# Optimization experiments

Hardware: AMD Instinct MI355X
Metric: run time of the kernel (lower is better)

Reference implementation:

```python
import jax, jax.numpy as jnp
import numpy as np
from jax import lax

B, M, D, N = 256, 1024, 128, 26  # batch, seq_len, feat_dim, num_labels


def setup_inputs() -> dict:
    key = jax.random.key(0)
    k1, k2, k3, k4 = jax.random.split(key, 4)
    X = jax.random.normal(k1, (B, M, D), dtype=jnp.float32)
    labels = jax.random.randint(k2, (B, M), 0, N, dtype=jnp.int32)
    # Learned CRF params (zeros in the module; random here for a non-degenerate test).
    W = jax.random.normal(k3, (N, D), dtype=jnp.float32) * 0.05
    T = jax.random.normal(k4, (N, N), dtype=jnp.float32) * 0.1
    return {"X": X, "labels": labels, "W": W, "T": T}


def _seq_log_prob(x, y, W, T):
    # x: [M, D], y: [M] int labels.
    # Original forward_messages (prob space): f[i,a] = exp(x_i.W_a) * sum_b exp(T[b,a]) f[i-1,b]
    # Computed here equivalently in log space for numerical stability.
    e = x @ W.T  # [M, N] emission scores x_i . W_a

    def step(lf, e_i):
        # logsumexp over previous label b of (lf[b] + T[b, a])
        lf_new = e_i + jax.nn.logsumexp(lf[:, None] + T, axis=0)
        return lf_new, None

    lf_last, _ = lax.scan(step, e[0], e[1:])
    logZ = jax.nn.logsumexp(lf_last)
    unnorm = jnp.sum(jnp.take_along_axis(e, y[:, None], axis=1)) \
        + jnp.sum(T[y[:-1], y[1:]])
    return unnorm - logZ


def reference(X, labels, W, T):
    # CRF.forward with identity conv stack: mean log p(y | x) over the batch.
    log_probs = jax.vmap(lambda x, y: _seq_log_prob(x, y, W, T))(X, labels)
    return jnp.mean(log_probs)
```

## Files before the change

### kernel.cpp

```cpp
#include <hip/hip_runtime.h>

#define CB 256
#define CM 1024
#define CD 128
#define CN 26

typedef __attribute__((ext_vector_type(2))) float f32x2;

__device__ inline float rfl_f(float x) {
    return __int_as_float(__builtin_amdgcn_readfirstlane(__float_as_int(x)));
}
__device__ inline float rdl_f(float x, int lane) {
#if __has_builtin(__builtin_amdgcn_readlane)
    return __int_as_float(__builtin_amdgcn_readlane(__float_as_int(x), lane));
#else
    return __shfl(x, lane, 64);
#endif
}
__device__ inline float fexp2(float x) {
#if __has_builtin(__builtin_amdgcn_exp2f)
    return __builtin_amdgcn_exp2f(x);
#else
    return exp2f(x);
#endif
}
__device__ inline float flog2(float x) {
#if __has_builtin(__builtin_amdgcn_logf)
    return __builtin_amdgcn_logf(x);
#else
    return log2f(x);
#endif
}
__device__ inline f32x2 fma2(f32x2 a, f32x2 b, f32x2 c) {
#if __has_builtin(__builtin_elementwise_fma)
    return __builtin_elementwise_fma(a, b, c);
#else
    f32x2 r;
    r[0] = fmaf(a[0], b[0], c[0]);
    r[1] = fmaf(a[1], b[1], c[1]);
    return r;
#endif
}

__global__ __launch_bounds__(256, 2) void emit_kernel(
    const float* __restrict__ X, const float* __restrict__ W,
    const int* __restrict__ labels, const float* __restrict__ T,
    float* __restrict__ E, float* __restrict__ out) {
    const int t = threadIdx.x;
    const int row = blockIdx.x * 256 + t;
    const float4* __restrict__ x4 =
        reinterpret_cast<const float4*>(X + (size_t)row * CD);

    f32x2 acc2[CN];
#pragma unroll
    for (int a = 0; a < CN; ++a) acc2[a] = (f32x2){0.f, 0.f};

    f32x2 xa[8], xb[8];
#pragma unroll
    for (int q = 0; q < 4; ++q)
        *reinterpret_cast<float4*>(&xa[q * 2]) = x4[q];

#pragma unroll
    for (int c = 0; c < 8; ++c) {
        f32x2* cur = (c & 1) ? xb : xa;
        f32x2* nxt = (c & 1) ? xa : xb;
        if (c < 7) {
#pragma unroll
            for (int q = 0; q < 4; ++q)
                *reinterpret_cast<float4*>(&nxt[q * 2]) = x4[(c + 1) * 4 + q];
        }
#pragma unroll
        for (int a = 0; a < CN; ++a) {
            const f32x2* wp =
                reinterpret_cast<const f32x2*>(W + a * CD + c * 16);
#pragma unroll
            for (int jj = 0; jj < 8; ++jj)
                acc2[a] = fma2(cur[jj], wp[jj], acc2[a]);
        }
    }

    float acc[CN];
#pragma unroll
    for (int a = 0; a < CN; ++a) acc[a] = acc2[a][0] + acc2[a][1];

    const float LOG2E = 1.4426950408889634f;
    float2* e2 = reinterpret_cast<float2*>(E + (size_t)row * CN);
#pragma unroll
    for (int a = 0; a < CN / 2; ++a)
        e2[a] = make_float2(acc[2 * a] * LOG2E, acc[2 * a + 1] * LOG2E);

    int y = labels[row];
    float us = acc[0];
#pragma unroll
    for (int a = 1; a < CN; ++a) us = (y == a) ? acc[a] : us;
    if (row & (CM - 1)) {
        int yp = labels[row - 1];
        us += T[yp * CN + y];
    }
#pragma unroll
    for (int off = 32; off > 0; off >>= 1) us += __shfl_xor(us, off, 64);
    __shared__ float rsum[4];
    if ((t & 63) == 0) rsum[t >> 6] = us;
    __syncthreads();
    if (t == 0)
        atomicAdd(out, (rsum[0] + rsum[1] + rsum[2] + rsum[3]) * (1.f / CB));
}

template <bool BWD>
__device__ void run_half(float* __restrict__ base, const float* __restrict__ T,
                         int a, int l) {
    float AT[CN];
#pragma unroll
    for (int k = 0; k < CN; ++k)
        AT[k] = expf(BWD ? T[a * CN + k] : T[k * CN + a]);

    const int S = BWD ? -CN : CN;
    const float* __restrict__ Eb = base + (BWD ? (size_t)1023 * CN : 0) + a;

    float f, L = 0.f;
    float epf[8];
    const float* pf;
    if (BWD) {
        f = 1.f;
#pragma unroll
        for (int k = 0; k < 8; ++k) epf[k] = Eb[k * S];
        pf = Eb + 8 * S;
    } else {
        f = fexp2(Eb[0]);
#pragma unroll
        for (int k = 0; k < 8; ++k) epf[k] = Eb[(1 + k) * S];
        pf = Eb + 9 * S;
    }

    auto step = [&](float e_cur, bool renorm) {
        float p = fexp2(e_cur);
        float x = BWD ? p * f : f;
        float d0 = 0.f, d1 = 0.f, d2 = 0.f, d3 = 0.f;
#pragma unroll
        for (int b = 0; b < 24; b += 4) {
            d0 = fmaf(AT[b + 0], rdl_f(x, b + 0), d0);
            d1 = fmaf(AT[b + 1], rdl_f(x, b + 1), d1);
            d2 = fmaf(AT[b + 2], rdl_f(x, b + 2), d2);
            d3 = fmaf(AT[b + 3], rdl_f(x, b + 3), d3);
        }
        d0 = fmaf(AT[24], rdl_f(x, 24), d0);
        d1 = fmaf(AT[25], rdl_f(x, 25), d1);
        float d = (d0 + d1) + (d2 + d3);
        f = BWD ? d : p * d;
        if (renorm) {
            float fr = rfl_f(f);
            int k2 = (int)((__float_as_uint(fr) >> 23) & 255) - 127;
            f = ldexpf(f, -k2);
            L += (float)k2;
        }
    };

    const int NMAIN = BWD ? 63 : 62;
    for (int it = 0; it < NMAIN; ++it) {
#pragma unroll
        for (int k = 0; k < 8; ++k) {
            float e_cur = epf[k];
            epf[k] = pf[k * S];
            step(e_cur, k == 7);
        }
        pf += 8 * S;
    }
    if (BWD) {
#pragma unroll
        for (int k = 0; k < 8; ++k) step(epf[k], k == 7);
    } else {
#pragma unroll
        for (int k = 0; k < 8; ++k) {
            float e_cur = epf[k];
            if (k < 7) epf[k] = pf[k * S];
            step(e_cur, k == 7);
        }
#pragma unroll
        for (int k = 0; k < 7; ++k) step(epf[k], false);
    }

    {
        float fr = rfl_f(f);
        int k2 = (int)((__float_as_uint(fr) >> 23) & 255) - 127;
        f = ldexpf(f, -k2);
        L += (float)k2;
    }

    base[(BWD ? (size_t)1023 * CN : 0) + a] = f;
    if (l == 0) base[(BWD ? (size_t)1022 * CN : (size_t)CN)] = L;
}

__global__ __launch_bounds__(64) void crf_half_kernel(
    float* __restrict__ E, const float* __restrict__ T) {
    const int s = blockIdx.x >> 1;
    const int l = threadIdx.x;
    const int a = (l < CN) ? l : (CN - 1);
    float* base = E + (size_t)s * CM * CN;
    if (blockIdx.x & 1)
        run_half<true>(base, T, a, l);
    else
        run_half<false>(base, T, a, l);
}

__global__ __launch_bounds__(64) void crf_combine_kernel(
    const float* __restrict__ E, float* __restrict__ out) {
    const int s = blockIdx.x;
    const int l = threadIdx.x;
    const float LN2 = 0.6931471805599453f;
    const float* base = E + (size_t)s * CM * CN;

    float v = 0.f;
    if (l < CN) v = base[l] * base[(size_t)1023 * CN + l];
#pragma unroll
    for (int off = 32; off > 0; off >>= 1) v += __shfl_xor(v, off, 64);

    if (l == 0) {
        float Lf = base[CN];
        float Lb = base[(size_t)1022 * CN];
        float logZ = LN2 * (Lf + Lb + flog2(v));
        atomicAdd(out, -logZ * (1.f / (float)CB));
    }
}

extern "C" void kernel_launch(void* const* d_in, const int* in_sizes, int n_in,
                              void* d_out, int out_size, void* d_ws,
                              size_t ws_size, hipStream_t stream) {
    const float* X = (const float*)d_in[0];
    const int* labels = (const int*)d_in[1];
    const float* W = (const float*)d_in[2];
    const float* T = (const float*)d_in[3];
    float* out = (float*)d_out;
    float* E = (float*)d_ws;

    hipMemsetAsync(d_out, 0, sizeof(float), stream);
    emit_kernel<<<(CB * CM) / 256, 256, 0, stream>>>(X, W, labels, T, E, out);
    crf_half_kernel<<<CB * 2, 64, 0, stream>>>(E, T);
    crf_combine_kernel<<<CB, 64, 0, stream>>>(E, out);
}
```

Measured before the change: 294.8 us.

## Stage W in LDS and compute four rows per thread in emission kernel

```diff
diff --git a/kernel.cpp b/kernel.cpp
--- a/kernel.cpp
+++ b/kernel.cpp
@@ -4,8 +4,6 @@
 #define CM 1024
 #define CD 128
 #define CN 26
-
-typedef __attribute__((ext_vector_type(2))) float f32x2;
 
 __device__ inline float rfl_f(float x) {
     return __int_as_float(__builtin_amdgcn_readfirstlane(__float_as_int(x)));
@@ -31,75 +29,85 @@
     return log2f(x);
 #endif
 }
-__device__ inline f32x2 fma2(f32x2 a, f32x2 b, f32x2 c) {
-#if __has_builtin(__builtin_elementwise_fma)
-    return __builtin_elementwise_fma(a, b, c);
-#else
-    f32x2 r;
-    r[0] = fmaf(a[0], b[0], c[0]);
-    r[1] = fmaf(a[1], b[1], c[1]);
-    return r;
-#endif
-}
-
-__global__ __launch_bounds__(256, 2) void emit_kernel(
+
+__global__ __launch_bounds__(256, 1) void emit_kernel(
     const float* __restrict__ X, const float* __restrict__ W,
     const int* __restrict__ labels, const float* __restrict__ T,
     float* __restrict__ E, float* __restrict__ out) {
+    __shared__ float Ws[CN * CD];
+    __shared__ float rsum[4];
+
     const int t = threadIdx.x;
-    const int row = blockIdx.x * 256 + t;
-    const float4* __restrict__ x4 =
-        reinterpret_cast<const float4*>(X + (size_t)row * CD);
-
-    f32x2 acc2[CN];
-#pragma unroll
-    for (int a = 0; a < CN; ++a) acc2[a] = (f32x2){0.f, 0.f};
-
-    f32x2 xa[8], xb[8];
-#pragma unroll
-    for (int q = 0; q < 4; ++q)
-        *reinterpret_cast<float4*>(&xa[q * 2]) = x4[q];
-
-#pragma unroll
-    for (int c = 0; c < 8; ++c) {
-        f32x2* cur = (c & 1) ? xb : xa;
-        f32x2* nxt = (c & 1) ? xa : xb;
-        if (c < 7) {
-#pragma unroll
-            for (int q = 0; q < 4; ++q)
-                *reinterpret_cast<float4*>(&nxt[q * 2]) = x4[(c + 1) * 4 + q];
+    const int row0 = blockIdx.x * 1024 + t * 4;
+
+    for (int i = t; i < CN * CD; i += 256) Ws[i] = W[i];
+    __syncthreads();
+
+    float acc[4][CN];
+#pragma unroll
+    for (int g = 0; g < 4; ++g)
+#pragma unroll
+        for (int a = 0; a < CN; ++a) acc[g][a] = 0.f;
+
+    const float4* __restrict__ x40 =
+        reinterpret_cast<const float4*>(X + (size_t)row0 * CD);
+    const float4* Ws4 = reinterpret_cast<const float4*>(Ws);
+
+#pragma unroll 1
+    for (int c = 0; c < 16; ++c) {
+        float4 xv[4][2];
+#pragma unroll
+        for (int g = 0; g < 4; ++g) {
+            xv[g][0] = x40[g * 32 + c * 2];
+            xv[g][1] = x40[g * 32 + c * 2 + 1];
         }
 #pragma unroll
         for (int a = 0; a < CN; ++a) {
-            const f32x2* wp =
-                reinterpret_cast<const f32x2*>(W + a * CD + c * 16);
-#pragma unroll
-            for (int jj = 0; jj < 8; ++jj)
-                acc2[a] = fma2(cur[jj], wp[jj], acc2[a]);
-        }
-    }
-
-    float acc[CN];
-#pragma unroll
-    for (int a = 0; a < CN; ++a) acc[a] = acc2[a][0] + acc2[a][1];
+            float4 w0 = Ws4[a * 32 + c * 2];
+            float4 w1 = Ws4[a * 32 + c * 2 + 1];
+#pragma unroll
+            for (int g = 0; g < 4; ++g) {
+                float s = acc[g][a];
+                s = fmaf(xv[g][0].x, w0.x, s);
+                s = fmaf(xv[g][0].y, w0.y, s);
+                s = fmaf(xv[g][0].z, w0.z, s);
+                s = fmaf(xv[g][0].w, w0.w, s);
+                s = fmaf(xv[g][1].x, w1.x, s);
+                s = fmaf(xv[g][1].y, w1.y, s);
+                s = fmaf(xv[g][1].z, w1.z, s);
+                s = fmaf(xv[g][1].w, w1.w, s);
+                acc[g][a] = s;
+            }
+        }
+    }
 
     const float LOG2E = 1.4426950408889634f;
-    float2* e2 = reinterpret_cast<float2*>(E + (size_t)row * CN);
-#pragma unroll
-    for (int a = 0; a < CN / 2; ++a)
-        e2[a] = make_float2(acc[2 * a] * LOG2E, acc[2 * a + 1] * LOG2E);
-
-    int y = labels[row];
-    float us = acc[0];
-#pragma unroll
-    for (int a = 1; a < CN; ++a) us = (y == a) ? acc[a] : us;
-    if (row & (CM - 1)) {
-        int yp = labels[row - 1];
-        us += T[yp * CN + y];
+#pragma unroll
+    for (int g = 0; g < 4; ++g) {
+        float2* e2 =
+            reinterpret_cast<float2*>(E + (size_t)(row0 + g) * CN);
+#pragma unroll
+        for (int a = 0; a < CN / 2; ++a)
+            e2[a] = make_float2(acc[g][2 * a] * LOG2E,
+                                acc[g][2 * a + 1] * LOG2E);
+    }
+
+    float us = 0.f;
+#pragma unroll
+    for (int g = 0; g < 4; ++g) {
+        int row = row0 + g;
+        int y = labels[row];
+        float sel = acc[g][0];
+#pragma unroll
+        for (int a = 1; a < CN; ++a) sel = (y == a) ? acc[g][a] : sel;
+        us += sel;
+        if (row & (CM - 1)) {
+            int yp = labels[row - 1];
+            us += T[yp * CN + y];
+        }
     }
 #pragma unroll
     for (int off = 32; off > 0; off >>= 1) us += __shfl_xor(us, off, 64);
-    __shared__ float rsum[4];
     if ((t & 63) == 0) rsum[t >> 6] = us;
     __syncthreads();
     if (t == 0)
@@ -233,7 +241,7 @@
     float* E = (float*)d_ws;
 
     hipMemsetAsync(d_out, 0, sizeof(float), stream);
-    emit_kernel<<<(CB * CM) / 256, 256, 0, stream>>>(X, W, labels, T, E, out);
+    emit_kernel<<<(CB * CM) / 1024, 256, 0, stream>>>(X, W, labels, T, E, out);
     crf_half_kernel<<<CB * 2, 64, 0, stream>>>(E, T);
     crf_combine_kernel<<<CB, 64, 0, stream>>>(E, out);
 }
```

After: 283.0 us. 4.0% less time.
